# Performance work log

Hardware: AMD Instinct MI355X
Metric: run time of the kernel (lower is better)

## Reference

```python
import math
import jax, jax.numpy as jnp
import numpy as np

B, T, C, H = 4, 2048, 1024, 16
D = C // H  # head dim = 64


def setup_inputs() -> dict:
    key = jax.random.key(0)
    k1, k2, k3 = jax.random.split(key, 3)
    scale = 1.0 / math.sqrt(C)
    return {
        "x": jax.random.normal(k1, (B, T, C), jnp.float32),
        "w_attn": jax.random.normal(k2, (C, 3 * C), jnp.float32) * scale,
        "b_attn": jnp.zeros((3 * C,), jnp.float32),
        "w_proj": jax.random.normal(k3, (C, C), jnp.float32) * scale,
        "b_proj": jnp.zeros((C,), jnp.float32),
    }


def reference(x, w_attn, b_attn, w_proj, b_proj):
    Bx, Tx, Cx = x.shape
    qkv = x @ w_attn + b_attn                       # [B,T,3C]
    q, k, v = jnp.split(qkv, 3, axis=-1)
    # [B,T,C] -> [B,H,T,D]
    q = q.reshape(Bx, Tx, H, D).transpose(0, 2, 1, 3)
    k = k.reshape(Bx, Tx, H, D).transpose(0, 2, 1, 3)
    v = v.reshape(Bx, Tx, H, D).transpose(0, 2, 1, 3)
    att = jnp.einsum('bhqd,bhkd->bhqk', q, k) * (1.0 / math.sqrt(D))
    causal = jnp.tril(jnp.ones((Tx, Tx), bool))     # [T,T]
    att = jnp.where(causal, att, -jnp.inf)
    att = jax.nn.softmax(att, axis=-1)
    y = jnp.einsum('bhqk,bhkd->bhqd', att, v)       # [B,H,T,D]
    y = y.transpose(0, 2, 1, 3).reshape(Bx, Tx, Cx)
    return y @ w_proj + b_proj
```

## Files before the change

### kernel.cpp

```cpp
#include <hip/hip_runtime.h>
#include <hip/hip_bf16.h>

typedef __bf16 bf16;
typedef __attribute__((ext_vector_type(4))) __bf16 bf16x4;
typedef __attribute__((ext_vector_type(8))) __bf16 bf16x8;
typedef __attribute__((ext_vector_type(4))) float f32x4;
typedef __attribute__((ext_vector_type(16))) float f32x16;
typedef __attribute__((ext_vector_type(2))) unsigned u32x2;
typedef __attribute__((ext_vector_type(4))) unsigned u32x4;

#define B_ 4
#define T_ 2048
#define C_ 1024
#define H_ 16
#define D_ 64
#define BT_ (B_*T_)

#define NEG_INF (-__builtin_inff())

__device__ __forceinline__ void gld16(const void* g, void* l) {
  __builtin_amdgcn_global_load_lds(
      (const __attribute__((address_space(1))) void*)g,
      (__attribute__((address_space(3))) void*)l, 16, 0, 0);
}

__device__ __forceinline__ unsigned cvtpk(float lo, float hi) {
  unsigned r;
  asm("v_cvt_pk_bf16_f32 %0, %1, %2" : "=v"(r) : "v"(lo), "v"(hi));
  return r;
}


__global__ void cast_x(const float* __restrict__ in, bf16* __restrict__ out) {
  int i = blockIdx.x * 256 + threadIdx.x;
  f32x4 v = reinterpret_cast<const f32x4*>(in)[i];
  bf16x4 o;
  o[0] = (bf16)v[0]; o[1] = (bf16)v[1]; o[2] = (bf16)v[2]; o[3] = (bf16)v[3];
  reinterpret_cast<bf16x4*>(out)[i] = o;
}

__global__ void transpose_cast(const float* __restrict__ in, bf16* __restrict__ out,
                               int R, int Cc) {
  __shared__ float tile[32][33];
  int tx = threadIdx.x, ty = threadIdx.y;
  int x  = blockIdx.x * 32 + tx;
  int y0 = blockIdx.y * 32;
#pragma unroll
  for (int j = 0; j < 32; j += 8)
    tile[ty + j][tx] = in[(size_t)(y0 + ty + j) * Cc + x];
  __syncthreads();
  int ox  = y0 + tx;
  int oy0 = blockIdx.x * 32;
#pragma unroll
  for (int j = 0; j < 32; j += 8)
    out[(size_t)(oy0 + ty + j) * R + ox] = (bf16)tile[tx][ty + j];
}


template<int EPI>
__global__ __launch_bounds__(512, 4)
void gemm_bt(const bf16* __restrict__ A, const bf16* __restrict__ Bt,
             const float* __restrict__ bias, float* __restrict__ outF,
             bf16* __restrict__ qb, bf16* __restrict__ kb, bf16* __restrict__ vb,
             int M, int N, int K) {
  __shared__ alignas(16) bf16 As[3][128 * 32];
  __shared__ alignas(16) bf16 Bs[3][256 * 32];
  const int tid = threadIdx.x;
  const int lane = tid & 63, wid = tid >> 6;
  const int wm = wid >> 2, wn = wid & 3;
  const int lr = lane & 15, lg = lane >> 4;

  const int nbx = gridDim.x;
  const int nwg = nbx * gridDim.y;
  const int bid = blockIdx.y * nbx + blockIdx.x;
  const int swz = (bid & 7) * (nwg >> 3) + (bid >> 3);
  const int m0 = (swz / nbx) * 128, n0 = (swz % nbx) * 256;

  f32x4 acc[4][4] = {};

#define GSTAGE(BF, KT) do {                                                    \
    int k0_ = (KT) << 5;                                                       \
    { int row_ = tid >> 2, ke_ = (tid & 3) << 3;                               \
      gld16(A + (size_t)(m0 + row_) * K + k0_ + ke_, As[BF] + tid * 8); }      \
    _Pragma("unroll")                                                          \
    for (int j_ = 0; j_ < 2; ++j_) {                                           \
      int s_ = j_ * 512 + tid;                                                 \
      int row_ = s_ >> 2, ke_ = (s_ & 3) << 3;                                 \
      gld16(Bt + (size_t)(n0 + row_) * K + k0_ + ke_, Bs[BF] + s_ * 8);        \
    }                                                                          \
  } while (0)

  const int ktiles = K >> 5;
  GSTAGE(0, 0);
  GSTAGE(1, 1);
  for (int kt = 0; kt < ktiles; ++kt) {
    if (kt + 1 < ktiles) asm volatile("s_waitcnt vmcnt(3)" ::: "memory");
    else                 asm volatile("s_waitcnt vmcnt(0)" ::: "memory");
    __builtin_amdgcn_s_barrier();
    asm volatile("" ::: "memory");
    if (kt + 2 < ktiles) GSTAGE((kt + 2) % 3, kt + 2);

    const bf16* Ac = As[kt % 3];
    const bf16* Bc = Bs[kt % 3];
    bf16x8 af[4], bfr[4];
#pragma unroll
    for (int i = 0; i < 4; i++)
      af[i]  = *(const bf16x8*)(Ac + ((wm * 64 + i * 16 + lr) << 5) + (lg << 3));
#pragma unroll
    for (int j = 0; j < 4; j++)
      bfr[j] = *(const bf16x8*)(Bc + ((wn * 64 + j * 16 + lr) << 5) + (lg << 3));
#pragma unroll
    for (int i = 0; i < 4; i++)
#pragma unroll
      for (int j = 0; j < 4; j++)
        acc[i][j] = __builtin_amdgcn_mfma_f32_16x16x32_bf16(af[i], bfr[j], acc[i][j], 0, 0, 0);
  }
#undef GSTAGE

  if (EPI == 1) {
#pragma unroll
    for (int i = 0; i < 4; i++) {
      int row = m0 + wm * 64 + i * 16 + lg * 4;
#pragma unroll
      for (int j = 0; j < 4; j++) {
        int col = n0 + wn * 64 + j * 16 + lr;
        float bv = bias[col];
#pragma unroll
        for (int r = 0; r < 4; r++)
          outF[(size_t)(row + r) * N + col] = acc[i][j][r] + bv;
      }
    }
  } else {
    const int sect = n0 >> 10;
#pragma unroll
    for (int i = 0; i < 4; i++) {
      int row = m0 + wm * 64 + i * 16 + lg * 4;
#pragma unroll
      for (int j = 0; j < 4; j++) {
        int col = n0 + wn * 64 + j * 16 + lr;
        float bv = bias[col];
        int cm = col & 1023;
        int h = cm >> 6, d = cm & 63;
#pragma unroll
        for (int r = 0; r < 4; r++) {
          float v = acc[i][j][r] + bv;
          int rt = row + r;
          int b = rt >> 11, t = rt & 2047;
          bf16 o = (bf16)v;
          size_t bh = (size_t)(b * H_ + h);
          if (sect == 0)      qb[(bh * T_ + t) * D_ + d] = o;
          else if (sect == 1) kb[(bh * T_ + t) * D_ + d] = o;
          else                vb[(bh * D_ + d) * T_ + t] = o;
        }
      }
    }
  }
}


#if __has_builtin(__builtin_amdgcn_permlane32_swap)
#define PERMSWAP(A, B, LOW, HIW) do {                                           \
    auto _r = __builtin_amdgcn_permlane32_swap((unsigned)(A), (unsigned)(B),    \
                                               false, false);                   \
    __builtin_memcpy(&(LOW), &_r, 4);                                           \
    __builtin_memcpy(&(HIW), (const char*)&_r + 4, 4);                          \
  } while (0)
#else
#define PERMSWAP(A, B, LOW, HIW) do {                                           \
    unsigned _sb = (unsigned)__shfl_xor((int)(B), 32, 64);                      \
    unsigned _sa = (unsigned)__shfl_xor((int)(A), 32, 64);                      \
    (LOW) = hi ? _sb : (A);                                                     \
    (HIW) = hi ? (B) : _sa;                                                     \
  } while (0)
#endif

__global__ __launch_bounds__(256, 4)
void attn_fwd(const bf16* __restrict__ qg, const bf16* __restrict__ kg,
              const bf16* __restrict__ vg, bf16* __restrict__ yb) {
  __shared__ alignas(16) bf16 Ks[3][64 * 64];
  __shared__ alignas(16) bf16 Vs[3][64 * 64];
  const int tid = threadIdx.x;
  const int lane = tid & 63, wid = tid >> 6;
  const int hi = lane >> 5, lq = lane & 31;
  const int xr = (lq & 7) << 4;
  const int bh = blockIdx.y;
  const int NQ = T_ / 128;

  const char* kbase = (const char*)(kg + (size_t)bh * T_ * D_);
  const char* vbase = (const char*)(vg + (size_t)bh * D_ * T_);
  const int b_ = bh >> 4, h = bh & 15;

#define STAGE(BF, TT) do {                                                     \
    _Pragma("unroll")                                                          \
    for (int j_ = 0; j_ < 2; ++j_) {                                           \
      int s_ = j_ * 256 + tid;                                                 \
      int row_ = s_ >> 3;                                                      \
      int scb_ = ((s_ & 7) << 4) ^ ((row_ & 7) << 4);                          \
      gld16(kbase + (size_t)((TT) * 64 + row_) * 128 + scb_,                   \
            (char*)Ks[BF] + s_ * 16);                                          \
      gld16(vbase + (size_t)row_ * (T_ * 2) + (TT) * 128 + scb_,               \
            (char*)Vs[BF] + s_ * 16);                                          \
    }                                                                          \
  } while (0)

  for (int ph = 0; ph < 2; ++ph) {
    const int qblk = ph ? (int)blockIdx.x : (NQ - 1 - (int)blockIdx.x);
    const int wq0 = qblk * 128 + wid * 32;
    const int qrow = wq0 + lq;
    const int nt = 2 * qblk + 2;

    if (ph) __builtin_amdgcn_s_barrier();
    STAGE(0, 0);
    STAGE(1, 1);

    const bf16* qptr = qg + ((size_t)bh * T_ + qrow) * D_ + hi * 8;
    bf16x8 qf[4];
#pragma unroll
    for (int s = 0; s < 4; s++) {
      qf[s] = *(const bf16x8*)(qptr + 16 * s);
      asm volatile("" : "+v"(qf[s]));
    }

    f32x16 o[2] = {};
    float mrow = NEG_INF, lrow = 0.f;

    for (int t = 0; t < nt; ++t) {
      if (t + 1 < nt) asm volatile("s_waitcnt vmcnt(4)" ::: "memory");
      else            asm volatile("s_waitcnt vmcnt(0)" ::: "memory");
      __builtin_amdgcn_s_barrier();
      asm volatile("" ::: "memory");
      if (t + 2 < nt) STAGE((t + 2) % 3, t + 2);

      const char* Kc = (const char*)Ks[t % 3];
      const char* Vc = (const char*)Vs[t % 3];

      f32x16 S[2] = {};
      __builtin_amdgcn_s_setprio(1);
#pragma unroll
      for (int s = 0; s < 4; s++) {
#pragma unroll
        for (int b = 0; b < 2; b++) {
          bf16x8 kf = *(const bf16x8*)(Kc + (b * 32 + lq) * 128 +
                                       ((32 * s + 16 * hi) ^ xr));
          S[b] = __builtin_amdgcn_mfma_f32_32x32x16_bf16(kf, qf[s], S[b], 0, 0, 0);
        }
      }
      __builtin_amdgcn_s_setprio(0);

      if (t >= nt - 2) {
#pragma unroll
        for (int b = 0; b < 2; b++)
#pragma unroll
          for (int r = 0; r < 16; r++) {
            int kgl = t * 64 + b * 32 + (r & 3) + 8 * (r >> 2) + 4 * hi;
            if (kgl > qrow) S[b][r] = NEG_INF;
          }
      }

      float tm = NEG_INF;
#pragma unroll
      for (int b = 0; b < 2; b++)
#pragma unroll
        for (int r = 0; r < 16; r++) tm = fmaxf(tm, S[b][r]);
      tm = fmaxf(tm, __shfl_xor(tm, 32, 64));

      float mn = fmaxf(mrow, 0.125f * tm);
      float alpha = __expf(mrow - mn);
      mrow = mn;
      float rs = 0.f;
#pragma unroll
      for (int b = 0; b < 2; b++)
#pragma unroll
        for (int r = 0; r < 16; r++) {
          float e = __expf(fmaf(S[b][r], 0.125f, -mn));
          S[b][r] = e;
          rs += e;
        }
      rs += __shfl_xor(rs, 32, 64);
      lrow = lrow * alpha + rs;
#pragma unroll
      for (int db = 0; db < 2; db++)
#pragma unroll
        for (int r = 0; r < 16; r++) o[db][r] *= alpha;

      __builtin_amdgcn_s_setprio(1);
#pragma unroll
      for (int ks = 0; ks < 4; ks++) {
        const int b = ks >> 1, hf = ks & 1;
        unsigned A0 = cvtpk(S[b][8 * hf + 0], S[b][8 * hf + 1]);
        unsigned A1 = cvtpk(S[b][8 * hf + 2], S[b][8 * hf + 3]);
        unsigned B0 = cvtpk(S[b][8 * hf + 4], S[b][8 * hf + 5]);
        unsigned B1 = cvtpk(S[b][8 * hf + 6], S[b][8 * hf + 7]);
        unsigned w0, w1, w2, w3;
        PERMSWAP(A0, B0, w0, w2);
        PERMSWAP(A1, B1, w1, w3);
        u32x4 wv = {w0, w1, w2, w3};
        bf16x8 pf = __builtin_bit_cast(bf16x8, wv);
#pragma unroll
        for (int db = 0; db < 2; db++) {
          bf16x8 vf = *(const bf16x8*)(Vc + (db * 32 + lq) * 128 +
                                       ((32 * ks + 16 * hi) ^ xr));
          o[db] = __builtin_amdgcn_mfma_f32_32x32x16_bf16(vf, pf, o[db], 0, 0, 0);
        }
      }
      __builtin_amdgcn_s_setprio(0);
    }

    float inv = 1.f / lrow;
    bf16* yrow = yb + ((size_t)(b_ * T_ + qrow)) * C_ + h * 64 + hi * 4;
#pragma unroll
    for (int db = 0; db < 2; db++)
#pragma unroll
      for (int rq = 0; rq < 4; rq++) {
        unsigned w0 = cvtpk(o[db][4 * rq + 0] * inv, o[db][4 * rq + 1] * inv);
        unsigned w1 = cvtpk(o[db][4 * rq + 2] * inv, o[db][4 * rq + 3] * inv);
        u32x2 wv = {w0, w1};
        *(u32x2*)(yrow + db * 32 + rq * 8) = wv;
      }
  }
#undef STAGE
}


extern "C" void kernel_launch(void* const* d_in, const int* in_sizes, int n_in,
                              void* d_out, int out_size, void* d_ws, size_t ws_size,
                              hipStream_t stream) {
  (void)in_sizes; (void)n_in; (void)out_size; (void)ws_size;
  const float* x      = (const float*)d_in[0];
  const float* w_attn = (const float*)d_in[1];
  const float* b_attn = (const float*)d_in[2];
  const float* w_proj = (const float*)d_in[3];
  const float* b_proj = (const float*)d_in[4];
  float* out = (float*)d_out;

  char* ws = (char*)d_ws;
  bf16* x_bf = (bf16*)ws;  ws += (size_t)BT_ * C_ * 2;
  bf16* wat  = (bf16*)ws;  ws += (size_t)3 * C_ * C_ * 2;
  bf16* wpt  = (bf16*)ws;  ws += (size_t)C_ * C_ * 2;
  bf16* qbuf = (bf16*)ws;  ws += (size_t)BT_ * C_ * 2;
  bf16* kbuf = (bf16*)ws;  ws += (size_t)BT_ * C_ * 2;
  bf16* vbuf = (bf16*)ws;  ws += (size_t)BT_ * C_ * 2;
  bf16* ybuf = (bf16*)ws;

  cast_x<<<(BT_ * C_ / 4) / 256, 256, 0, stream>>>(x, x_bf);
  transpose_cast<<<dim3(3 * C_ / 32, C_ / 32), dim3(32, 8), 0, stream>>>(w_attn, wat, C_, 3 * C_);
  transpose_cast<<<dim3(C_ / 32, C_ / 32), dim3(32, 8), 0, stream>>>(w_proj, wpt, C_, C_);

  gemm_bt<0><<<dim3(3 * C_ / 256, BT_ / 128), 512, 0, stream>>>(
      x_bf, wat, b_attn, nullptr, qbuf, kbuf, vbuf, BT_, 3 * C_, C_);

  attn_fwd<<<dim3(T_ / 256, B_ * H_), 256, 0, stream>>>(qbuf, kbuf, vbuf, ybuf);

  gemm_bt<1><<<dim3(C_ / 256, BT_ / 128), 512, 0, stream>>>(
      ybuf, wpt, b_proj, out, nullptr, nullptr, nullptr, BT_, C_, C_);
}
```

Baseline: 307.9 us.

## Swizzle GEMM LDS layout, remap tiles per XCD, raise MFMA priority

Applies an XOR swizzle to the k-chunk position of each row when loading A and B tiles into LDS, and reads fragments with the matching swizzled offset. This removes LDS bank conflicts in the ds_read of bf16x8 fragments. The block-to-tile mapping now gives each group of blocks (bid & 7) a contiguous range of M rows, which is meant to improve L2 reuse per XCD. The MFMA loop is also wrapped in s_setprio so waves issuing matrix ops get scheduling priority.

```diff
diff --git a/kernel.cpp b/kernel.cpp
--- a/kernel.cpp
+++ b/kernel.cpp
@@ -69,24 +69,29 @@
   const int lane = tid & 63, wid = tid >> 6;
   const int wm = wid >> 2, wn = wid & 3;
   const int lr = lane & 15, lg = lane >> 4;
+  const int fx = (lr ^ (lr >> 2)) & 3;
+  const int koff = (lg ^ fx) << 3;
 
   const int nbx = gridDim.x;
-  const int nwg = nbx * gridDim.y;
   const int bid = blockIdx.y * nbx + blockIdx.x;
-  const int swz = (bid & 7) * (nwg >> 3) + (bid >> 3);
-  const int m0 = (swz / nbx) * 128, n0 = (swz % nbx) * 256;
+  const int x = bid & 7, j = bid >> 3;
+  const int mpx = gridDim.y >> 3;
+  const int m0 = (x * mpx + j % mpx) * 128;
+  const int n0 = (j / mpx) * 256;
 
   f32x4 acc[4][4] = {};
 
 #define GSTAGE(BF, KT) do {                                                    \
     int k0_ = (KT) << 5;                                                       \
-    { int row_ = tid >> 2, ke_ = (tid & 3) << 3;                               \
-      gld16(A + (size_t)(m0 + row_) * K + k0_ + ke_, As[BF] + tid * 8); }      \
+    { int row_ = tid >> 2, sl_ = tid & 3;                                      \
+      int gs_ = sl_ ^ ((row_ ^ (row_ >> 2)) & 3);                              \
+      gld16(A + (size_t)(m0 + row_) * K + k0_ + (gs_ << 3), As[BF] + tid * 8); }\
     _Pragma("unroll")                                                          \
     for (int j_ = 0; j_ < 2; ++j_) {                                           \
       int s_ = j_ * 512 + tid;                                                 \
-      int row_ = s_ >> 2, ke_ = (s_ & 3) << 3;                                 \
-      gld16(Bt + (size_t)(n0 + row_) * K + k0_ + ke_, Bs[BF] + s_ * 8);        \
+      int row_ = s_ >> 2, sl_ = s_ & 3;                                        \
+      int gs_ = sl_ ^ ((row_ ^ (row_ >> 2)) & 3);                              \
+      gld16(Bt + (size_t)(n0 + row_) * K + k0_ + (gs_ << 3), Bs[BF] + s_ * 8); \
     }                                                                          \
   } while (0)
 
@@ -105,15 +110,17 @@
     bf16x8 af[4], bfr[4];
 #pragma unroll
     for (int i = 0; i < 4; i++)
-      af[i]  = *(const bf16x8*)(Ac + ((wm * 64 + i * 16 + lr) << 5) + (lg << 3));
-#pragma unroll
-    for (int j = 0; j < 4; j++)
-      bfr[j] = *(const bf16x8*)(Bc + ((wn * 64 + j * 16 + lr) << 5) + (lg << 3));
+      af[i]  = *(const bf16x8*)(Ac + ((wm * 64 + i * 16 + lr) << 5) + koff);
+#pragma unroll
+    for (int j2 = 0; j2 < 4; j2++)
+      bfr[j2] = *(const bf16x8*)(Bc + ((wn * 64 + j2 * 16 + lr) << 5) + koff);
+    __builtin_amdgcn_s_setprio(1);
 #pragma unroll
     for (int i = 0; i < 4; i++)
 #pragma unroll
-      for (int j = 0; j < 4; j++)
-        acc[i][j] = __builtin_amdgcn_mfma_f32_16x16x32_bf16(af[i], bfr[j], acc[i][j], 0, 0, 0);
+      for (int j2 = 0; j2 < 4; j2++)
+        acc[i][j2] = __builtin_amdgcn_mfma_f32_16x16x32_bf16(af[i], bfr[j2], acc[i][j2], 0, 0, 0);
+    __builtin_amdgcn_s_setprio(0);
   }
 #undef GSTAGE
 
@@ -122,12 +129,12 @@
     for (int i = 0; i < 4; i++) {
       int row = m0 + wm * 64 + i * 16 + lg * 4;
 #pragma unroll
-      for (int j = 0; j < 4; j++) {
-        int col = n0 + wn * 64 + j * 16 + lr;
+      for (int j2 = 0; j2 < 4; j2++) {
+        int col = n0 + wn * 64 + j2 * 16 + lr;
         float bv = bias[col];
 #pragma unroll
         for (int r = 0; r < 4; r++)
-          outF[(size_t)(row + r) * N + col] = acc[i][j][r] + bv;
+          outF[(size_t)(row + r) * N + col] = acc[i][j2][r] + bv;
       }
     }
   } else {
@@ -136,14 +143,14 @@
     for (int i = 0; i < 4; i++) {
       int row = m0 + wm * 64 + i * 16 + lg * 4;
 #pragma unroll
-      for (int j = 0; j < 4; j++) {
-        int col = n0 + wn * 64 + j * 16 + lr;
+      for (int j2 = 0; j2 < 4; j2++) {
+        int col = n0 + wn * 64 + j2 * 16 + lr;
         float bv = bias[col];
         int cm = col & 1023;
         int h = cm >> 6, d = cm & 63;
 #pragma unroll
         for (int r = 0; r < 4; r++) {
-          float v = acc[i][j][r] + bv;
+          float v = acc[i][j2][r] + bv;
           int rt = row + r;
           int b = rt >> 11, t = rt & 2047;
           bf16 o = (bf16)v;
```

Result: faster. 289.0 us (-6.2%).

## Retile GEMM to 256x128x64 with XOR-swizzled LDS and per-XCD tile mapping

Applied to the files above, without the earlier changes.

Changes the GEMM block tile from 128x256 with K-step 32 to 256x128 with K-step 64. LDS staging now uses an XOR swizzle to avoid bank conflicts, and workgroups are remapped so each XCD gets contiguous M rows. MFMA sections are wrapped in setprio. The aim is to cut barrier and loop overhead per K, reduce LDS conflicts and improve L2 locality. In exchange, LDS use per block doubles (144KB for three stages) and occupancy drops to 2 per the launch bounds.

```diff
diff --git a/kernel.cpp b/kernel.cpp
--- a/kernel.cpp
+++ b/kernel.cpp
@@ -58,43 +58,48 @@
 
 
 template<int EPI>
-__global__ __launch_bounds__(512, 4)
+__global__ __launch_bounds__(512, 2)
 void gemm_bt(const bf16* __restrict__ A, const bf16* __restrict__ Bt,
              const float* __restrict__ bias, float* __restrict__ outF,
              bf16* __restrict__ qb, bf16* __restrict__ kb, bf16* __restrict__ vb,
              int M, int N, int K) {
-  __shared__ alignas(16) bf16 As[3][128 * 32];
-  __shared__ alignas(16) bf16 Bs[3][256 * 32];
+  __shared__ alignas(16) bf16 As[3][256 * 64];
+  __shared__ alignas(16) bf16 Bs[3][128 * 64];
   const int tid = threadIdx.x;
   const int lane = tid & 63, wid = tid >> 6;
   const int wm = wid >> 2, wn = wid & 3;
   const int lr = lane & 15, lg = lane >> 4;
 
   const int nbx = gridDim.x;
-  const int nwg = nbx * gridDim.y;
   const int bid = blockIdx.y * nbx + blockIdx.x;
-  const int swz = (bid & 7) * (nwg >> 3) + (bid >> 3);
-  const int m0 = (swz / nbx) * 128, n0 = (swz % nbx) * 256;
-
-  f32x4 acc[4][4] = {};
+  const int xcd = bid & 7, j = bid >> 3;
+  const int mpx = gridDim.y >> 3;
+  const int m0 = (xcd * mpx + j % mpx) * 256;
+  const int n0 = (j / mpx) * 128;
+
+  f32x4 acc[8][2] = {};
 
 #define GSTAGE(BF, KT) do {                                                    \
-    int k0_ = (KT) << 5;                                                       \
-    { int row_ = tid >> 2, ke_ = (tid & 3) << 3;                               \
-      gld16(A + (size_t)(m0 + row_) * K + k0_ + ke_, As[BF] + tid * 8); }      \
+    const size_t kk_ = (size_t)(KT) * 64;                                      \
+    _Pragma("unroll")                                                          \
+    for (int j_ = 0; j_ < 4; ++j_) {                                           \
+      int S_ = j_ * 512 + tid;                                                 \
+      int row_ = S_ >> 3, sl_ = (S_ & 7) ^ (row_ & 7);                         \
+      gld16(A + (size_t)(m0 + row_) * K + kk_ + (sl_ << 3), As[BF] + S_ * 8);  \
+    }                                                                          \
     _Pragma("unroll")                                                          \
     for (int j_ = 0; j_ < 2; ++j_) {                                           \
-      int s_ = j_ * 512 + tid;                                                 \
-      int row_ = s_ >> 2, ke_ = (s_ & 3) << 3;                                 \
-      gld16(Bt + (size_t)(n0 + row_) * K + k0_ + ke_, Bs[BF] + s_ * 8);        \
+      int S_ = j_ * 512 + tid;                                                 \
+      int row_ = S_ >> 3, sl_ = (S_ & 7) ^ (row_ & 7);                         \
+      gld16(Bt + (size_t)(n0 + row_) * K + kk_ + (sl_ << 3), Bs[BF] + S_ * 8); \
     }                                                                          \
   } while (0)
 
-  const int ktiles = K >> 5;
+  const int ktiles = K >> 6;
   GSTAGE(0, 0);
   GSTAGE(1, 1);
   for (int kt = 0; kt < ktiles; ++kt) {
-    if (kt + 1 < ktiles) asm volatile("s_waitcnt vmcnt(3)" ::: "memory");
+    if (kt + 1 < ktiles) asm volatile("s_waitcnt vmcnt(6)" ::: "memory");
     else                 asm volatile("s_waitcnt vmcnt(0)" ::: "memory");
     __builtin_amdgcn_s_barrier();
     asm volatile("" ::: "memory");
@@ -102,48 +107,71 @@
 
     const bf16* Ac = As[kt % 3];
     const bf16* Bc = Bs[kt % 3];
-    bf16x8 af[4], bfr[4];
-#pragma unroll
-    for (int i = 0; i < 4; i++)
-      af[i]  = *(const bf16x8*)(Ac + ((wm * 64 + i * 16 + lr) << 5) + (lg << 3));
-#pragma unroll
-    for (int j = 0; j < 4; j++)
-      bfr[j] = *(const bf16x8*)(Bc + ((wn * 64 + j * 16 + lr) << 5) + (lg << 3));
-#pragma unroll
-    for (int i = 0; i < 4; i++)
-#pragma unroll
-      for (int j = 0; j < 4; j++)
-        acc[i][j] = __builtin_amdgcn_mfma_f32_16x16x32_bf16(af[i], bfr[j], acc[i][j], 0, 0, 0);
+
+    bf16x8 bfr[2][2];
+#pragma unroll
+    for (int j2 = 0; j2 < 2; j2++) {
+      int row = wn * 32 + j2 * 16 + lr;
+#pragma unroll
+      for (int s = 0; s < 2; s++) {
+        int slot = (s * 4 + lg) ^ (row & 7);
+        bfr[j2][s] = *(const bf16x8*)(Bc + (row << 6) + (slot << 3));
+      }
+    }
+#pragma unroll
+    for (int mh = 0; mh < 2; mh++) {
+      bf16x8 af[4][2];
+#pragma unroll
+      for (int i = 0; i < 4; i++) {
+        int row = wm * 128 + mh * 64 + i * 16 + lr;
+#pragma unroll
+        for (int s = 0; s < 2; s++) {
+          int slot = (s * 4 + lg) ^ (row & 7);
+          af[i][s] = *(const bf16x8*)(Ac + (row << 6) + (slot << 3));
+        }
+      }
+      __builtin_amdgcn_s_setprio(1);
+#pragma unroll
+      for (int i = 0; i < 4; i++)
+#pragma unroll
+        for (int j2 = 0; j2 < 2; j2++) {
+          f32x4 a = acc[mh * 4 + i][j2];
+          a = __builtin_amdgcn_mfma_f32_16x16x32_bf16(af[i][0], bfr[j2][0], a, 0, 0, 0);
+          a = __builtin_amdgcn_mfma_f32_16x16x32_bf16(af[i][1], bfr[j2][1], a, 0, 0, 0);
+          acc[mh * 4 + i][j2] = a;
+        }
+      __builtin_amdgcn_s_setprio(0);
+    }
   }
 #undef GSTAGE
 
   if (EPI == 1) {
 #pragma unroll
-    for (int i = 0; i < 4; i++) {
-      int row = m0 + wm * 64 + i * 16 + lg * 4;
-#pragma unroll
-      for (int j = 0; j < 4; j++) {
-        int col = n0 + wn * 64 + j * 16 + lr;
+    for (int a = 0; a < 8; a++) {
+      int row = m0 + wm * 128 + a * 16 + lg * 4;
+#pragma unroll
+      for (int j2 = 0; j2 < 2; j2++) {
+        int col = n0 + wn * 32 + j2 * 16 + lr;
         float bv = bias[col];
 #pragma unroll
         for (int r = 0; r < 4; r++)
-          outF[(size_t)(row + r) * N + col] = acc[i][j][r] + bv;
+          outF[(size_t)(row + r) * N + col] = acc[a][j2][r] + bv;
       }
     }
   } else {
     const int sect = n0 >> 10;
 #pragma unroll
-    for (int i = 0; i < 4; i++) {
-      int row = m0 + wm * 64 + i * 16 + lg * 4;
-#pragma unroll
-      for (int j = 0; j < 4; j++) {
-        int col = n0 + wn * 64 + j * 16 + lr;
+    for (int a = 0; a < 8; a++) {
+      int row = m0 + wm * 128 + a * 16 + lg * 4;
+#pragma unroll
+      for (int j2 = 0; j2 < 2; j2++) {
+        int col = n0 + wn * 32 + j2 * 16 + lr;
         float bv = bias[col];
         int cm = col & 1023;
         int h = cm >> 6, d = cm & 63;
 #pragma unroll
         for (int r = 0; r < 4; r++) {
-          float v = acc[i][j][r] + bv;
+          float v = acc[a][j2][r] + bv;
           int rt = row + r;
           int b = rt >> 11, t = rt & 2047;
           bf16 o = (bf16)v;
@@ -346,11 +374,11 @@
   transpose_cast<<<dim3(3 * C_ / 32, C_ / 32), dim3(32, 8), 0, stream>>>(w_attn, wat, C_, 3 * C_);
   transpose_cast<<<dim3(C_ / 32, C_ / 32), dim3(32, 8), 0, stream>>>(w_proj, wpt, C_, C_);
 
-  gemm_bt<0><<<dim3(3 * C_ / 256, BT_ / 128), 512, 0, stream>>>(
+  gemm_bt<0><<<dim3(3 * C_ / 128, BT_ / 256), 512, 0, stream>>>(
       x_bf, wat, b_attn, nullptr, qbuf, kbuf, vbuf, BT_, 3 * C_, C_);
 
   attn_fwd<<<dim3(T_ / 256, B_ * H_), 256, 0, stream>>>(qbuf, kbuf, vbuf, ybuf);
 
-  gemm_bt<1><<<dim3(C_ / 256, BT_ / 128), 512, 0, stream>>>(
+  gemm_bt<1><<<dim3(C_ / 128, BT_ / 256), 512, 0, stream>>>(
       ybuf, wpt, b_proj, out, nullptr, nullptr, nullptr, BT_, C_, C_);
 }
```

Result: faster. 288.9 us (-6.2%).
